# Kernel optimization log

Hardware: AMD Instinct MI355X
Metric: run time of the kernel (lower is better)

Reference implementation:

```python
import jax, jax.numpy as jnp
import numpy as np

B, C, T = 8, 64, 128

def _conv(x, w, b, stride=1, pad=1, groups=1):
    y = jax.lax.conv_general_dilated(x, w, (stride, stride), [(pad, pad), (pad, pad)],
                                     feature_group_count=groups,
                                     dimension_numbers=('NCHW', 'OIHW', 'NCHW'))
    return y + b[None, :, None, None]

def _lrelu(x):
    return jnp.where(x > 0, x, 0.1 * x)

def _ps4(A, Bt, Ct, Dt):
    # qiancha(A,B,C,D) interleaves channels with stride 4; PixelShuffle(2) then maps
    # group index j in [0..3] to pixel offset (j//2, j%2): A->(0,0), B->(0,1), C->(1,0), D->(1,1)
    b, c, h, w = A.shape
    s = jnp.stack([A, Bt, Ct, Dt], axis=2).reshape(b, c, 2, 2, h, w)
    return s.transpose(0, 1, 4, 2, 5, 3).reshape(b, c, 2 * h, 2 * w)

def _il2(A, Bt):
    # qiancha2: stride-2 channel interleave
    b, c, h, w = A.shape
    return jnp.stack([A, Bt], axis=2).reshape(b, 2 * c, h, w)

def setup_inputs():
    key = jax.random.key(0)
    ks = jax.random.split(key, 20)
    def w(k, shape):
        return 0.05 * jax.random.normal(k, shape, dtype=jnp.float32)
    d = {}
    d['x'] = jax.random.normal(ks[0], (B, C, T, T), dtype=jnp.float32)
    d['w_hwc'] = w(ks[1], (3 * C, C, 1, 1)); d['b_hwc'] = w(ks[2], (3 * C,))
    d['w_dw'] = w(ks[3], (3 * C, 1, 3, 3)); d['b_dw'] = w(ks[4], (3 * C,))
    d['w_hw'] = w(ks[5], (C, C, 3, 3)); d['b_hw'] = w(ks[6], (C,))
    d['w_cw'] = w(ks[7], (T, T, 3, 3)); d['b_cw'] = w(ks[8], (T,))
    d['w_hc'] = w(ks[9], (T, T, 3, 3)); d['b_hc'] = w(ks[10], (T,))
    d['w_down'] = w(ks[11], (C, 2 * C, 2, 2)); d['b_down'] = w(ks[12], (C,))
    d['w_l1'] = w(ks[13], (C, C, 3, 3)); d['b_l1'] = w(ks[14], (C,))
    d['w_l2'] = w(ks[15], (C, C, 3, 3)); d['b_l2'] = w(ks[16], (C,))
    return d

def reference(x, w_hwc, b_hwc, w_dw, b_dw, w_hw, b_hw, w_cw, b_cw, w_hc, b_hc,
              w_down, b_down, w_l1, b_l1, w_l2, b_l2):
    c = x.shape[1]
    # 1x1 expand then depthwise 3x3 -> three gating maps
    hwc = _conv(_conv(x, w_hwc, b_hwc, pad=0), w_dw, b_dw, pad=1, groups=3 * c)
    HW, CW, HC = jnp.split(hwc, 3, axis=1)
    x_hw = _lrelu(_conv(x, w_hw, b_hw)) * HW
    x_cw = _lrelu(_conv(x.transpose(0, 2, 1, 3), w_cw, b_cw)).transpose(0, 2, 1, 3) * CW
    x_hc = _lrelu(_conv(x.transpose(0, 3, 2, 1), w_hc, b_hc)).transpose(0, 3, 2, 1) * HC
    xqc1 = _ps4(x, x_hw, x_cw, x_hc)
    xqc2 = _ps4(x_hc, x_cw, x_hw, x)
    xqc = _il2(xqc1, xqc2)                              # [B, 2C, 2T, 2T]
    out = _conv(xqc, w_down, b_down, stride=2, pad=0) + x
    out1 = _lrelu(_conv(out, w_l1, b_l1))
    out1 = _lrelu(_conv(out1, w_l2, b_l2))
    return x + out1
```

## Files before the change

### kernel.cpp

```cpp
#include <hip/hip_runtime.h>
#include <hip/hip_bf16.h>

#define BB 8
#define CC 64
#define TT 128
#define PP (TT*TT)
#define C3 192

typedef __hip_bfloat16 bf16;
typedef __attribute__((ext_vector_type(8))) short short8;
typedef __attribute__((ext_vector_type(4))) float floatx4;

__device__ __forceinline__ float b2f(bf16 v){ return __bfloat162float(v); }
__device__ __forceinline__ bf16 f2b(float v){ return __float2bfloat16(v); }
__device__ __forceinline__ short8 lds8(const bf16* p){ return *(const short8*)(const void*)p; }

__global__ void k_wpk(const float* __restrict__ w_down, const float* __restrict__ w_hc,
                      const float* __restrict__ w_cw,  const float* __restrict__ w_hwc,
                      const float* __restrict__ w_hw,  const float* __restrict__ w_l1,
                      const float* __restrict__ w_l2,  const float* __restrict__ w_dw,
                      const float* __restrict__ b_hwc, const float* __restrict__ b_dw,
                      bf16* __restrict__ wpkd,
                      bf16* __restrict__ wpkhw, bf16* __restrict__ wpkl1,
                      bf16* __restrict__ wpkl2, bf16* __restrict__ wpkcw,
                      bf16* __restrict__ wpkhc, bf16* __restrict__ wpkg,
                      float* __restrict__ bg){
  int i = blockIdx.x*256 + threadIdx.x;
  if (i < 147456){
    int j = i & 7, lane = (i>>3) & 63, mm = (i>>9) & 7, kk = (i>>12) & 3, t = i >> 14;
    int m = mm*16 + (lane & 15);
    int k = kk*32 + (lane>>4)*8 + j;
    wpkcw[i] = f2b(w_cw[m*1152 + k*9 + t]);
    wpkhc[i] = f2b(w_hc[m*1152 + k*9 + t]);
  }
  if (i < 36864){
    int j = i & 7, lane = (i>>3) & 63, mm = (i>>9) & 3, kk = (i>>11) & 1, t = i >> 12;
    int oc = mm*16 + (lane & 15);
    int ic = kk*32 + (lane>>4)*8 + j;
    int s = oc*576 + ic*9 + t;
    wpkhw[i] = f2b(w_hw[s]);
    wpkl1[i] = f2b(w_l1[s]);
    wpkl2[i] = f2b(w_l2[s]);
  }
  if (i < 110592){
    int j = i & 7, lane = (i>>3) & 63, rest = i >> 9;
    int mm = rest % 12, tk = rest / 12;
    int oc = mm*16 + (lane & 15);
    int ic = (tk & 1)*32 + (lane>>4)*8 + j;
    int t = tk >> 1;
    wpkg[i] = f2b(w_dw[oc*9 + t] * w_hwc[oc*64 + ic]);
  }
  if (i < 1728){
    int cls = i / C3, oc = i % C3;
    int ch = cls / 3, cw = cls % 3;
    float S = 0.f;
    for (int dh = (ch==0?1:0); dh <= (ch==2?1:2); ++dh)
      for (int dw = (cw==0?1:0); dw <= (cw==2?1:2); ++dw)
        S += w_dw[oc*9 + dh*3 + dw];
    bg[cls*C3 + oc] = b_dw[oc] + b_hwc[oc]*S;
  }
  if (i < 16384){
    int j = i & 7, lane = (i>>3) & 63, mm = (i>>9) & 3, kk = i >> 11;
    int m = mm*16 + (lane & 15);
    int k = kk*32 + (lane>>4)*8 + j;
    int s = k >> 6, c = k & 63;
    wpkd[i] = f2b(w_down[m*512 + c*8 + s] + w_down[m*512 + c*8 + 7 - s]);
  }
}

__global__ void k_pack(const float* __restrict__ x, bf16* __restrict__ xh,
                       bf16* __restrict__ xb16){
  int h = blockIdx.x, b = blockIdx.y;
  __shared__ float xs[64][129];
  for (int idx = threadIdx.x; idx < 2048; idx += 256){
    int c = idx >> 5, w4 = (idx & 31)*4;
    float4 v = *(const float4*)(x + ((size_t)b*CC + c)*PP + h*TT + w4);
    bf16 o4[4] = { f2b(v.x), f2b(v.y), f2b(v.z), f2b(v.w) };
    *(uint2*)(xb16 + ((size_t)b*CC + c)*PP + h*TT + w4) = *(uint2*)o4;
    xs[c][w4] = v.x; xs[c][w4+1] = v.y; xs[c][w4+2] = v.z; xs[c][w4+3] = v.w;
  }
  __syncthreads();
  for (int idx = threadIdx.x; idx < 8192; idx += 256){
    int w = idx >> 6, c = idx & 63;
    xh[(((size_t)b*TT + h)*TT + w)*64 + c] = f2b(xs[c][w]);
  }
}

__global__ void k_xw(const bf16* __restrict__ xb16, bf16* __restrict__ xW){
  int c = blockIdx.x, b = blockIdx.y;
  __shared__ unsigned short xs2[32][140];
  const bf16* src = xb16 + ((size_t)b*CC + c)*PP;
  unsigned short* dst = (unsigned short*)(xW + ((size_t)b*CC + c)*PP);
  for (int s = 0; s < 4; ++s){
    if (s) __syncthreads();
    for (int idx = threadIdx.x; idx < 512; idx += 256){
      int hl = idx >> 4, w8 = (idx & 15)*8;
      unsigned short tmp[8];
      *(uint4*)tmp = *(const uint4*)(src + (s*32 + hl)*TT + w8);
      #pragma unroll
      for (int j = 0; j < 8; ++j) xs2[hl][w8+j] = tmp[j];
    }
    __syncthreads();
    for (int idx = threadIdx.x; idx < 4096; idx += 256){
      int w = idx >> 5, hl = idx & 31;
      dst[w*TT + s*32 + hl] = xs2[hl][w];
    }
  }
}

__global__ __launch_bounds__(256)
void k_ghwm(const bf16* __restrict__ xh, const bf16* __restrict__ wpkg,
            const bf16* __restrict__ wpkhw, const float* __restrict__ bg,
            const float* __restrict__ b_hw, bf16* __restrict__ xhwh,
            bf16* __restrict__ g, int NB){
  int L = blockIdx.x;
  int b = L % NB; int r0 = L / NB;
  int h = r0 % TT; int w0b = (r0 / TT)*64;
  int tid = threadIdx.x, lane = tid & 63, wv = tid >> 6;
  int nlo = lane & 15, quad = lane >> 4;
  __shared__ bf16 xs[3][66][64];
  for (int idx = tid; idx < 1584; idx += 256){
    int dh = idx / 528, rr = idx % 528, wi = rr >> 3, ch = rr & 7;
    int gh = h + dh - 1, gw = w0b + wi - 1;
    uint4 v = make_uint4(0,0,0,0);
    if (gh >= 0 && gh < TT && gw >= 0 && gw < TT)
      v = *(const uint4*)(xh + (((size_t)b*TT + gh)*TT + gw)*64 + ch*8);
    *(uint4*)(&xs[dh][wi][((ch ^ (wi & 7)))*8]) = v;
  }
  __syncthreads();
  floatx4 acc[4][4] = {};
  #pragma unroll
  for (int t = 0; t < 9; ++t){
    int dh = t/3, dw = t%3;
    int swk = (nlo + dw) & 7;
    #pragma unroll
    for (int kk = 0; kk < 2; ++kk){
      int pc = ((kk*4 + quad) ^ swk)*8;
      short8 bfv[4];
      #pragma unroll
      for (int nn = 0; nn < 4; ++nn)
        bfv[nn] = lds8(&xs[dh][nn*16 + nlo + dw][pc]);
      short8 a0 = *(const short8*)(const void*)(wpkhw + (((t*2+kk)*4  + wv   )*64 + lane)*8);
      short8 a1 = *(const short8*)(const void*)(wpkg  + (((t*2+kk)*12 + wv   )*64 + lane)*8);
      short8 a2 = *(const short8*)(const void*)(wpkg  + (((t*2+kk)*12 + 4+wv )*64 + lane)*8);
      short8 a3 = *(const short8*)(const void*)(wpkg  + (((t*2+kk)*12 + 8+wv )*64 + lane)*8);
      #pragma unroll
      for (int nn = 0; nn < 4; ++nn){
        acc[0][nn] = __builtin_amdgcn_mfma_f32_16x16x32_bf16(a0, bfv[nn], acc[0][nn], 0,0,0);
        acc[1][nn] = __builtin_amdgcn_mfma_f32_16x16x32_bf16(a1, bfv[nn], acc[1][nn], 0,0,0);
        acc[2][nn] = __builtin_amdgcn_mfma_f32_16x16x32_bf16(a2, bfv[nn], acc[2][nn], 0,0,0);
        acc[3][nn] = __builtin_amdgcn_mfma_f32_16x16x32_bf16(a3, bfv[nn], acc[3][nn], 0,0,0);
      }
    }
  }
  int ch_cls3 = ((h == 0) ? 0 : (h == TT-1) ? 2 : 1)*3;
  int oc0 = wv*16 + quad*4;
  float4 bhw = *(const float4*)(b_hw + oc0);
  #pragma unroll
  for (int nn = 0; nn < 4; ++nn){
    int w = w0b + nn*16 + nlo;
    int cw_cls = (w == 0) ? 0 : (w == TT-1) ? 2 : 1;
    const float* bgrow = bg + (ch_cls3 + cw_cls)*C3;
    float4 bg0 = *(const float4*)(bgrow + oc0);
    float bga[4] = { bg0.x, bg0.y, bg0.z, bg0.w };
    float bha[4] = { bhw.x, bhw.y, bhw.z, bhw.w };
    bf16 o4[4];
    #pragma unroll
    for (int r = 0; r < 4; ++r){
      float hv = acc[0][nn][r] + bha[r];
      hv = hv > 0.f ? hv : 0.1f*hv;
      float gv = b2f(f2b(acc[1][nn][r] + bga[r]));
      o4[r] = f2b(hv * gv);
    }
    *(uint2*)(xhwh + (((size_t)b*PP + h*TT + w))*64 + oc0) = *(uint2*)o4;
  }
  __syncthreads();
  bf16* tb = &xs[0][0][0];
  #pragma unroll
  for (int p = 0; p < 2; ++p){
    #pragma unroll
    for (int nn = 0; nn < 4; ++nn){
      int wl = nn*16 + nlo;
      int w = w0b + wl;
      int cw_cls = (w == 0) ? 0 : (w == TT-1) ? 2 : 1;
      float4 bgp = *(const float4*)(bg + (ch_cls3 + cw_cls)*C3 + 64 + p*64 + oc0);
      float bga[4] = { bgp.x, bgp.y, bgp.z, bgp.w };
      #pragma unroll
      for (int r = 0; r < 4; ++r)
        tb[(p*64 + oc0 + r)*72 + wl] = f2b(acc[2+p][nn][r] + bga[r]);
    }
  }
  __syncthreads();
  #pragma unroll
  for (int i = 0; i < 4; ++i){
    int idx = i*256 + tid;
    int row = idx >> 3, wc = (idx & 7)*8;
    uint4 v = *(const uint4*)(tb + row*72 + wc);
    *(uint4*)(g + ((size_t)b*C3 + 64 + row)*PP + h*TT + w0b + wc) = v;
  }
}

__global__ __launch_bounds__(256)
void k_c3x3m(const bf16* __restrict__ in, const bf16* __restrict__ wpk,
             const float* __restrict__ bias,
             const float* __restrict__ resx, bf16* __restrict__ yb,
             float* __restrict__ yf, int mode, int NB){
  int L = blockIdx.x;
  int b = L % NB, h = L / NB;
  int tid = threadIdx.x, lane = tid & 63, wv = tid >> 6;
  int nlo = lane & 15, quad = lane >> 4;
  __shared__ bf16 xs[3][130][64];
  for (int idx = tid; idx < 3120; idx += 256){
    int dh = idx / 1040, r = idx % 1040, wi = r >> 3, ch = r & 7;
    int gh = h + dh - 1, gw = wi - 1;
    uint4 v = make_uint4(0,0,0,0);
    if (gh >= 0 && gh < TT && gw >= 0 && gw < TT)
      v = *(const uint4*)(in + (((size_t)b*TT + gh)*TT + gw)*64 + ch*8);
    *(uint4*)(&xs[dh][wi][((ch ^ (wi & 7)))*8]) = v;
  }
  __syncthreads();
  floatx4 acc[8] = {};
  #pragma unroll
  for (int t = 0; t < 9; ++t){
    int dh = t/3, dw = t%3;
    int swk = (nlo + dw) & 7;
    #pragma unroll
    for (int kk = 0; kk < 2; ++kk){
      short8 a = *(const short8*)(const void*)(wpk + (((t*2+kk)*4+wv)*64 + lane)*8);
      int pc = ((kk*4 + quad) ^ swk)*8;
      #pragma unroll
      for (int nn = 0; nn < 8; ++nn){
        short8 bf = lds8(&xs[dh][nn*16 + nlo + dw][pc]);
        acc[nn] = __builtin_amdgcn_mfma_f32_16x16x32_bf16(a, bf, acc[nn], 0,0,0);
      }
    }
  }
  int oc0 = wv*16 + quad*4;
  float4 bs = *(const float4*)(bias + oc0);
  float bsa[4] = { bs.x, bs.y, bs.z, bs.w };
  #pragma unroll
  for (int nn = 0; nn < 8; ++nn){
    int w = nn*16 + nlo;
    int pi = h*TT + w;
    if (mode == 1){
      bf16 o4[4];
      #pragma unroll
      for (int r = 0; r < 4; ++r){
        float v = acc[nn][r] + bsa[r];
        o4[r] = f2b(v > 0.f ? v : 0.1f*v);
      }
      *(uint2*)(yb + ((size_t)b*PP + pi)*64 + oc0) = *(uint2*)o4;
    } else {
      #pragma unroll
      for (int r = 0; r < 4; ++r){
        int oc = oc0 + r;
        float v = acc[nn][r] + bsa[r];
        v = v > 0.f ? v : 0.1f*v;
        yf[((size_t)b*CC + oc)*PP + pi] = v + resx[((size_t)b*CC + oc)*PP + pi];
      }
    }
  }
}

__global__ __launch_bounds__(256)
void k_cwm(const bf16* __restrict__ xW, const bf16* __restrict__ wpkcw,
           const float* __restrict__ bias, const bf16* __restrict__ g,
           bf16* __restrict__ xcw, int NB){
  int L = blockIdx.x;
  int b = L % NB; int r0 = L / NB;
  int c = r0 % CC; int w0b = (r0 / CC)*64;
  int tid = threadIdx.x, lane = tid & 63, wv = tid >> 6;
  int nlo = lane & 15, quad = lane >> 4;
  __shared__ bf16 xs[66][128];
  floatx4 acc[2][4] = {};
  for (int dc = 0; dc < 3; ++dc){
    int cc = c + dc - 1;
    if (cc < 0 || cc >= CC) continue;
    __syncthreads();
    for (int idx = tid; idx < 1056; idx += 256){
      int s = idx >> 4, ch = idx & 15;
      int gw = w0b - 1 + s;
      uint4 v = make_uint4(0,0,0,0);
      if (gw >= 0 && gw < TT)
        v = *(const uint4*)(xW + (((size_t)b*CC + cc)*TT + gw)*TT + ch*8);
      *(uint4*)(&xs[s][((ch ^ (s & 7)))*8]) = v;
    }
    __syncthreads();
    #pragma unroll
    for (int dw = 0; dw < 3; ++dw){
      int t = dc*3 + dw;
      int swk = (nlo + dw) & 7;
      #pragma unroll
      for (int kk = 0; kk < 4; ++kk){
        short8 a0 = *(const short8*)(const void*)(wpkcw + (((t*4+kk)*8 + wv*2    )*64 + lane)*8);
        short8 a1 = *(const short8*)(const void*)(wpkcw + (((t*4+kk)*8 + wv*2 + 1)*64 + lane)*8);
        int pc = ((kk*4 + quad) ^ swk)*8;
        #pragma unroll
        for (int nn = 0; nn < 4; ++nn){
          short8 bf = lds8(&xs[nn*16 + nlo + dw][pc]);
          acc[0][nn] = __builtin_amdgcn_mfma_f32_16x16x32_bf16(a0, bf, acc[0][nn], 0,0,0);
          acc[1][nn] = __builtin_amdgcn_mfma_f32_16x16x32_bf16(a1, bf, acc[1][nn], 0,0,0);
        }
      }
    }
  }
  #pragma unroll
  for (int ml = 0; ml < 2; ++ml){
    int ho0 = (wv*2 + ml)*16 + quad*4;
    float4 bs = *(const float4*)(bias + ho0);
    float bsa[4] = { bs.x, bs.y, bs.z, bs.w };
    #pragma unroll
    for (int nn = 0; nn < 4; ++nn){
      int w = w0b + nn*16 + nlo;
      #pragma unroll
      for (int r = 0; r < 4; ++r){
        int ho = ho0 + r;
        float v = acc[ml][nn][r] + bsa[r];
        v = v > 0.f ? v : 0.1f*v;
        v *= b2f(g[((size_t)b*C3 + 64 + c)*PP + ho*TT + w]);
        xcw[((size_t)b*CC + c)*PP + ho*TT + w] = f2b(v);
      }
    }
  }
}

__global__ __launch_bounds__(256)
void k_hcm(const bf16* __restrict__ xb16, const bf16* __restrict__ wpkhc,
           const float* __restrict__ bias, const bf16* __restrict__ g,
           bf16* __restrict__ xhch, int NB){
  int L = blockIdx.x;
  int b = L % NB, h = L / NB;
  int tid = threadIdx.x, lane = tid & 63, wv = tid >> 6;
  int nlo = lane & 15, quad = lane >> 4;
  __shared__ bf16 xs[66][128];
  floatx4 acc[2][4] = {};
  for (int dh = 0; dh < 3; ++dh){
    int gh = h + dh - 1;
    __syncthreads();
    for (int idx = tid; idx < 1056; idx += 256){
      int s = idx >> 4, ch = idx & 15;
      int cc = s - 1;
      uint4 v = make_uint4(0,0,0,0);
      if (cc >= 0 && cc < CC && gh >= 0 && gh < TT)
        v = *(const uint4*)(xb16 + (((size_t)b*CC + cc)*TT + gh)*TT + ch*8);
      *(uint4*)(&xs[s][((ch ^ (s & 7)))*8]) = v;
    }
    __syncthreads();
    #pragma unroll
    for (int dc = 0; dc < 3; ++dc){
      int t = dh*3 + dc;
      int swk = (nlo + dc) & 7;
      #pragma unroll
      for (int kk = 0; kk < 4; ++kk){
        short8 a0 = *(const short8*)(const void*)(wpkhc + (((t*4+kk)*8 + wv*2    )*64 + lane)*8);
        short8 a1 = *(const short8*)(const void*)(wpkhc + (((t*4+kk)*8 + wv*2 + 1)*64 + lane)*8);
        int pc = ((kk*4 + quad) ^ swk)*8;
        #pragma unroll
        for (int nn = 0; nn < 4; ++nn){
          short8 bf = lds8(&xs[nn*16 + nlo + dc][pc]);
          acc[0][nn] = __builtin_amdgcn_mfma_f32_16x16x32_bf16(a0, bf, acc[0][nn], 0,0,0);
          acc[1][nn] = __builtin_amdgcn_mfma_f32_16x16x32_bf16(a1, bf, acc[1][nn], 0,0,0);
        }
      }
    }
  }
  #pragma unroll
  for (int ml = 0; ml < 2; ++ml){
    int wo0 = (wv*2 + ml)*16 + quad*4;
    float4 bs = *(const float4*)(bias + wo0);
    float bsa[4] = { bs.x, bs.y, bs.z, bs.w };
    #pragma unroll
    for (int nn = 0; nn < 4; ++nn){
      int c = nn*16 + nlo;
      bf16 gg[4];
      *(uint2*)gg = *(const uint2*)(g + ((size_t)b*C3 + 128 + c)*PP + h*TT + wo0);
      #pragma unroll
      for (int r = 0; r < 4; ++r){
        float v = acc[ml][nn][r] + bsa[r];
        v = v > 0.f ? v : 0.1f*v;
        xhch[((size_t)b*PP + h*TT + wo0 + r)*64 + c] = f2b(v * b2f(gg[r]));
      }
    }
  }
}

__global__ __launch_bounds__(256)
void k_downm(const bf16* __restrict__ xh, const bf16* __restrict__ xhwh,
             const bf16* __restrict__ xcwn, const bf16* __restrict__ xhch,
             const bf16* __restrict__ wpkd, const float* __restrict__ x,
             const float* __restrict__ bias, bf16* __restrict__ outh){
  int h = blockIdx.x, b = blockIdx.y;
  int tid = threadIdx.x, lane = tid & 63, wv = tid >> 6;
  int nlo = lane & 15, quad = lane >> 4;
  int p0 = h*TT;
  __shared__ bf16 xs[128][76];
  for (int idx = tid; idx < 1024; idx += 256){
    int c = idx >> 4, w8 = (idx & 15)*8;
    bf16 tmp[8];
    *(uint4*)tmp = *(const uint4*)(xcwn + ((size_t)b*CC + c)*PP + p0 + w8);
    #pragma unroll
    for (int j = 0; j < 8; ++j) xs[w8+j][c] = tmp[j];
  }
  __syncthreads();
  int n0 = wv*32;
  floatx4 acc[4][2] = {};
  #pragma unroll
  for (int kk = 0; kk < 8; ++kk){
    int s = kk >> 1;
    int ko = (kk & 1)*32 + quad*8;
    short8 bfr[2];
    #pragma unroll
    for (int nn = 0; nn < 2; ++nn){
      int p = n0 + nn*16 + nlo;
      if (s == 2){
        bfr[nn] = lds8(&xs[p][ko]);
      } else {
        const bf16* src = (s == 0) ? xh : (s == 1) ? xhwh : xhch;
        bfr[nn] = *(const short8*)(const void*)(src + ((size_t)b*PP + p0 + p)*64 + ko);
      }
    }
    #pragma unroll
    for (int mm = 0; mm < 4; ++mm){
      short8 a = *(const short8*)(const void*)(wpkd + ((kk*4+mm)*64 + lane)*8);
      acc[mm][0] = __builtin_amdgcn_mfma_f32_16x16x32_bf16(a, bfr[0], acc[mm][0], 0,0,0);
      acc[mm][1] = __builtin_amdgcn_mfma_f32_16x16x32_bf16(a, bfr[1], acc[mm][1], 0,0,0);
    }
  }
  #pragma unroll
  for (int mm = 0; mm < 4; ++mm){
    int o0 = mm*16 + quad*4;
    float4 bs = *(const float4*)(bias + o0);
    float bsa[4] = { bs.x, bs.y, bs.z, bs.w };
    #pragma unroll
    for (int nn = 0; nn < 2; ++nn){
      int p = n0 + nn*16 + nlo;
      bf16 o4[4];
      #pragma unroll
      for (int r = 0; r < 4; ++r){
        float v = acc[mm][nn][r] + bsa[r] + x[((size_t)b*CC + o0 + r)*PP + p0 + p];
        o4[r] = f2b(v);
      }
      *(uint2*)(outh + ((size_t)b*PP + p0 + p)*64 + o0) = *(uint2*)o4;
    }
  }
}

extern "C" void kernel_launch(void* const* d_in, const int* in_sizes, int n_in,
                              void* d_out, int out_size, void* d_ws, size_t ws_size,
                              hipStream_t stream) {
  const float* x      = (const float*)d_in[0];
  const float* w_hwc  = (const float*)d_in[1];
  const float* b_hwc  = (const float*)d_in[2];
  const float* w_dw   = (const float*)d_in[3];
  const float* b_dw   = (const float*)d_in[4];
  const float* w_hw   = (const float*)d_in[5];
  const float* b_hw   = (const float*)d_in[6];
  const float* w_cw   = (const float*)d_in[7];
  const float* b_cw   = (const float*)d_in[8];
  const float* w_hc   = (const float*)d_in[9];
  const float* b_hc   = (const float*)d_in[10];
  const float* w_down = (const float*)d_in[11];
  const float* b_down = (const float*)d_in[12];
  const float* w_l1   = (const float*)d_in[13];
  const float* b_l1   = (const float*)d_in[14];
  const float* w_l2   = (const float*)d_in[15];
  const float* b_l2   = (const float*)d_in[16];
  float* out = (float*)d_out;

  char* ws = (char*)d_ws;
  bf16*  wpkd  = (bf16*) (ws + 0);
  float* bg    = (float*)(ws + 36864);
  bf16*  wpkhw = (bf16*) (ws + 65536);
  bf16*  wpkl1 = (bf16*) (ws + 139264);
  bf16*  wpkl2 = (bf16*) (ws + 212992);
  bf16*  wpkcw = (bf16*) (ws + 294912);
  bf16*  wpkhc = (bf16*) (ws + 589824);
  bf16*  wpkg  = (bf16*) (ws + 884736);

  k_wpk<<<576, 256, 0, stream>>>(w_down, w_hc, w_cw, w_hwc, w_hw, w_l1, w_l2,
                                 w_dw, b_hwc, b_dw,
                                 wpkd, wpkhw, wpkl1, wpkl2, wpkcw, wpkhc,
                                 wpkg, bg);

  if (ws_size >= 153092096ull) {
    bf16* g    = (bf16*)(ws + 2097152);
    bf16* xh   = (bf16*)(ws + 52428800);
    bf16* xW   = (bf16*)(ws + 69206016);
    bf16* xb16 = (bf16*)(ws + 85983232);
    bf16* xhwh = (bf16*)(ws + 102760448);
    bf16* xcw  = (bf16*)(ws + 119537664);
    bf16* xhch = (bf16*)(ws + 136314880);
    bf16* outh = xW;
    bf16* o1h  = xb16;

    k_pack<<<dim3(TT, BB), 256, 0, stream>>>(x, xh, xb16);
    k_xw<<<dim3(CC, BB), 256, 0, stream>>>(xb16, xW);
    k_ghwm<<<2*TT*BB, 256, 0, stream>>>(xh, wpkg, wpkhw, bg, b_hw, xhwh, g, BB);
    k_cwm  <<<2*CC*BB, 256, 0, stream>>>(xW, wpkcw, b_cw, g, xcw, BB);
    k_hcm  <<<TT*BB, 256, 0, stream>>>(xb16, wpkhc, b_hc, g, xhch, BB);
    k_downm<<<dim3(TT, BB), 256, 0, stream>>>(xh, xhwh, xcw, xhch, wpkd, x, b_down, outh);
    k_c3x3m<<<TT*BB, 256, 0, stream>>>(outh, wpkl1, b_l1, nullptr, o1h, nullptr, 1, BB);
    k_c3x3m<<<TT*BB, 256, 0, stream>>>(o1h, wpkl2, b_l2, x, nullptr, out, 2, BB);
  } else {
    char* P = ws + 2097152;
    bf16* g_b    = (bf16*)(P);
    bf16* xh_b   = (bf16*)(P + 6291456);
    bf16* xW_b   = (bf16*)(P + 8388608);
    bf16* xb_b   = (bf16*)(P + 10485760);
    bf16* xhwh_b = (bf16*)(P + 12582912);
    bf16* xcw_b  = (bf16*)(P + 14680064);
    bf16* xhch_b = (bf16*)(P + 16777216);
    bf16* outh_b = xW_b;
    bf16* o1h_b  = xb_b;
    for (int b = 0; b < BB; ++b){
      const float* xb = x + (size_t)b*CC*PP;
      float* outb = out + (size_t)b*CC*PP;
      k_pack<<<dim3(TT, 1), 256, 0, stream>>>(xb, xh_b, xb_b);
      k_xw<<<dim3(CC, 1), 256, 0, stream>>>(xb_b, xW_b);
      k_ghwm<<<2*TT, 256, 0, stream>>>(xh_b, wpkg, wpkhw, bg, b_hw, xhwh_b, g_b, 1);
      k_cwm  <<<2*CC, 256, 0, stream>>>(xW_b, wpkcw, b_cw, g_b, xcw_b, 1);
      k_hcm  <<<TT, 256, 0, stream>>>(xb_b, wpkhc, b_hc, g_b, xhch_b, 1);
      k_downm<<<dim3(TT, 1), 256, 0, stream>>>(xh_b, xhwh_b, xcw_b, xhch_b, wpkd, xb, b_down, outh_b);
      k_c3x3m<<<TT, 256, 0, stream>>>(outh_b, wpkl1, b_l1, nullptr, o1h_b, nullptr, 1, 1);
      k_c3x3m<<<TT, 256, 0, stream>>>(o1h_b, wpkl2, b_l2, xb, nullptr, outb, 2, 1);
    }
  }
}
```

Before: 287.0 us.

## Repartition MFMA warp tiles to cut LDS B-fragment reads in conv kernels

In three MFMA convolution kernels, each wave now owns a 2-D tile (more output-channel rows, fewer pixel columns) instead of a full row strip across all pixels. Each wave loads only 2 B fragments from LDS per k-step and reuses them across 4 A fragments read from global/L2 weights. Before, it loaded 4-8 B fragments per k-step. This lowers LDS read traffic per MFMA, at the cost of more global weight loads per wave.

```diff
diff --git a/kernel.cpp b/kernel.cpp
--- a/kernel.cpp
+++ b/kernel.cpp
@@ -219,44 +219,51 @@
     *(uint4*)(&xs[dh][wi][((ch ^ (wi & 7)))*8]) = v;
   }
   __syncthreads();
-  floatx4 acc[8] = {};
+  floatx4 acc[4][2] = {};
   #pragma unroll
   for (int t = 0; t < 9; ++t){
     int dh = t/3, dw = t%3;
     int swk = (nlo + dw) & 7;
     #pragma unroll
     for (int kk = 0; kk < 2; ++kk){
-      short8 a = *(const short8*)(const void*)(wpk + (((t*2+kk)*4+wv)*64 + lane)*8);
       int pc = ((kk*4 + quad) ^ swk)*8;
-      #pragma unroll
-      for (int nn = 0; nn < 8; ++nn){
-        short8 bf = lds8(&xs[dh][nn*16 + nlo + dw][pc]);
-        acc[nn] = __builtin_amdgcn_mfma_f32_16x16x32_bf16(a, bf, acc[nn], 0,0,0);
-      }
-    }
-  }
-  int oc0 = wv*16 + quad*4;
-  float4 bs = *(const float4*)(bias + oc0);
-  float bsa[4] = { bs.x, bs.y, bs.z, bs.w };
-  #pragma unroll
-  for (int nn = 0; nn < 8; ++nn){
-    int w = nn*16 + nlo;
-    int pi = h*TT + w;
-    if (mode == 1){
-      bf16 o4[4];
-      #pragma unroll
-      for (int r = 0; r < 4; ++r){
-        float v = acc[nn][r] + bsa[r];
-        o4[r] = f2b(v > 0.f ? v : 0.1f*v);
-      }
-      *(uint2*)(yb + ((size_t)b*PP + pi)*64 + oc0) = *(uint2*)o4;
-    } else {
-      #pragma unroll
-      for (int r = 0; r < 4; ++r){
-        int oc = oc0 + r;
-        float v = acc[nn][r] + bsa[r];
-        v = v > 0.f ? v : 0.1f*v;
-        yf[((size_t)b*CC + oc)*PP + pi] = v + resx[((size_t)b*CC + oc)*PP + pi];
+      short8 bfv[2];
+      #pragma unroll
+      for (int nn = 0; nn < 2; ++nn)
+        bfv[nn] = lds8(&xs[dh][wv*32 + nn*16 + nlo + dw][pc]);
+      #pragma unroll
+      for (int mm = 0; mm < 4; ++mm){
+        short8 a = *(const short8*)(const void*)(wpk + (((t*2+kk)*4+mm)*64 + lane)*8);
+        acc[mm][0] = __builtin_amdgcn_mfma_f32_16x16x32_bf16(a, bfv[0], acc[mm][0], 0,0,0);
+        acc[mm][1] = __builtin_amdgcn_mfma_f32_16x16x32_bf16(a, bfv[1], acc[mm][1], 0,0,0);
+      }
+    }
+  }
+  #pragma unroll
+  for (int mm = 0; mm < 4; ++mm){
+    int oc0 = mm*16 + quad*4;
+    float4 bs = *(const float4*)(bias + oc0);
+    float bsa[4] = { bs.x, bs.y, bs.z, bs.w };
+    #pragma unroll
+    for (int nn = 0; nn < 2; ++nn){
+      int w = wv*32 + nn*16 + nlo;
+      int pi = h*TT + w;
+      if (mode == 1){
+        bf16 o4[4];
+        #pragma unroll
+        for (int r = 0; r < 4; ++r){
+          float v = acc[mm][nn][r] + bsa[r];
+          o4[r] = f2b(v > 0.f ? v : 0.1f*v);
+        }
+        *(uint2*)(yb + ((size_t)b*PP + pi)*64 + oc0) = *(uint2*)o4;
+      } else {
+        #pragma unroll
+        for (int r = 0; r < 4; ++r){
+          int oc = oc0 + r;
+          float v = acc[mm][nn][r] + bsa[r];
+          v = v > 0.f ? v : 0.1f*v;
+          yf[((size_t)b*CC + oc)*PP + pi] = v + resx[((size_t)b*CC + oc)*PP + pi];
+        }
       }
     }
   }
@@ -270,9 +277,10 @@
   int b = L % NB; int r0 = L / NB;
   int c = r0 % CC; int w0b = (r0 / CC)*64;
   int tid = threadIdx.x, lane = tid & 63, wv = tid >> 6;
+  int mg = wv & 1, ng = wv >> 1;
   int nlo = lane & 15, quad = lane >> 4;
   __shared__ bf16 xs[66][128];
-  floatx4 acc[2][4] = {};
+  floatx4 acc[4][2] = {};
   for (int dc = 0; dc < 3; ++dc){
     int cc = c + dc - 1;
     if (cc < 0 || cc >= CC) continue;
@@ -292,26 +300,28 @@
       int swk = (nlo + dw) & 7;
       #pragma unroll
       for (int kk = 0; kk < 4; ++kk){
-        short8 a0 = *(const short8*)(const void*)(wpkcw + (((t*4+kk)*8 + wv*2    )*64 + lane)*8);
-        short8 a1 = *(const short8*)(const void*)(wpkcw + (((t*4+kk)*8 + wv*2 + 1)*64 + lane)*8);
         int pc = ((kk*4 + quad) ^ swk)*8;
+        short8 bfv[2];
         #pragma unroll
-        for (int nn = 0; nn < 4; ++nn){
-          short8 bf = lds8(&xs[nn*16 + nlo + dw][pc]);
-          acc[0][nn] = __builtin_amdgcn_mfma_f32_16x16x32_bf16(a0, bf, acc[0][nn], 0,0,0);
-          acc[1][nn] = __builtin_amdgcn_mfma_f32_16x16x32_bf16(a1, bf, acc[1][nn], 0,0,0);
+        for (int nn = 0; nn < 2; ++nn)
+          bfv[nn] = lds8(&xs[(ng*2+nn)*16 + nlo + dw][pc]);
+        #pragma unroll
+        for (int ml = 0; ml < 4; ++ml){
+          short8 a = *(const short8*)(const void*)(wpkcw + (((t*4+kk)*8 + mg*4 + ml)*64 + lane)*8);
+          acc[ml][0] = __builtin_amdgcn_mfma_f32_16x16x32_bf16(a, bfv[0], acc[ml][0], 0,0,0);
+          acc[ml][1] = __builtin_amdgcn_mfma_f32_16x16x32_bf16(a, bfv[1], acc[ml][1], 0,0,0);
         }
       }
     }
   }
   #pragma unroll
-  for (int ml = 0; ml < 2; ++ml){
-    int ho0 = (wv*2 + ml)*16 + quad*4;
+  for (int ml = 0; ml < 4; ++ml){
+    int ho0 = (mg*4 + ml)*16 + quad*4;
     float4 bs = *(const float4*)(bias + ho0);
     float bsa[4] = { bs.x, bs.y, bs.z, bs.w };
     #pragma unroll
-    for (int nn = 0; nn < 4; ++nn){
-      int w = w0b + nn*16 + nlo;
+    for (int nn = 0; nn < 2; ++nn){
+      int w = w0b + (ng*2+nn)*16 + nlo;
       #pragma unroll
       for (int r = 0; r < 4; ++r){
         int ho = ho0 + r;
@@ -331,9 +341,10 @@
   int L = blockIdx.x;
   int b = L % NB, h = L / NB;
   int tid = threadIdx.x, lane = tid & 63, wv = tid >> 6;
+  int mg = wv & 1, ng = wv >> 1;
   int nlo = lane & 15, quad = lane >> 4;
   __shared__ bf16 xs[66][128];
-  floatx4 acc[2][4] = {};
+  floatx4 acc[4][2] = {};
   for (int dh = 0; dh < 3; ++dh){
     int gh = h + dh - 1;
     __syncthreads();
@@ -352,26 +363,28 @@
       int swk = (nlo + dc) & 7;
       #pragma unroll
       for (int kk = 0; kk < 4; ++kk){
-        short8 a0 = *(const short8*)(const void*)(wpkhc + (((t*4+kk)*8 + wv*2    )*64 + lane)*8);
-        short8 a1 = *(const short8*)(const void*)(wpkhc + (((t*4+kk)*8 + wv*2 + 1)*64 + lane)*8);
         int pc = ((kk*4 + quad) ^ swk)*8;
+        short8 bfv[2];
         #pragma unroll
-        for (int nn = 0; nn < 4; ++nn){
-          short8 bf = lds8(&xs[nn*16 + nlo + dc][pc]);
-          acc[0][nn] = __builtin_amdgcn_mfma_f32_16x16x32_bf16(a0, bf, acc[0][nn], 0,0,0);
-          acc[1][nn] = __builtin_amdgcn_mfma_f32_16x16x32_bf16(a1, bf, acc[1][nn], 0,0,0);
+        for (int nn = 0; nn < 2; ++nn)
+          bfv[nn] = lds8(&xs[(ng*2+nn)*16 + nlo + dc][pc]);
+        #pragma unroll
+        for (int ml = 0; ml < 4; ++ml){
+          short8 a = *(const short8*)(const void*)(wpkhc + (((t*4+kk)*8 + mg*4 + ml)*64 + lane)*8);
+          acc[ml][0] = __builtin_amdgcn_mfma_f32_16x16x32_bf16(a, bfv[0], acc[ml][0], 0,0,0);
+          acc[ml][1] = __builtin_amdgcn_mfma_f32_16x16x32_bf16(a, bfv[1], acc[ml][1], 0,0,0);
         }
       }
     }
   }
   #pragma unroll
-  for (int ml = 0; ml < 2; ++ml){
-    int wo0 = (wv*2 + ml)*16 + quad*4;
+  for (int ml = 0; ml < 4; ++ml){
+    int wo0 = (mg*4 + ml)*16 + quad*4;
     float4 bs = *(const float4*)(bias + wo0);
     float bsa[4] = { bs.x, bs.y, bs.z, bs.w };
     #pragma unroll
-    for (int nn = 0; nn < 4; ++nn){
-      int c = nn*16 + nlo;
+    for (int nn = 0; nn < 2; ++nn){
+      int c = (ng*2+nn)*16 + nlo;
       bf16 gg[4];
       *(uint2*)gg = *(const uint2*)(g + ((size_t)b*C3 + 128 + c)*PP + h*TT + wo0);
       #pragma unroll
```

Result: slower. 328.9 us (+14.6%).
